# Kernel optimization log

Hardware: AMD Instinct MI355X
Metric: run time of the kernel (lower is better)

## Reference

```python
import jax, jax.numpy as jnp
import numpy as np

N_NODES = 100_000
N_EDGES = 1_600_000
N_GRAPHS = 512
NF = 64        # n_node_feats
H1 = 128       # hidden width
H2 = 64        # dim_node_emb
DIM_OUT = 1
STEPS = 4      # set2set processing steps


def _lin(x, W, b):
    # torch Linear convention: y = x @ W.T + b, W: [out, in]
    return x @ W.T + b


def _gelu(x):
    return jax.nn.gelu(x, approximate=False)  # torch.nn.GELU default (erf)


def _lstm_cell(x, h, c, Wih, Whh, bih, bhh):
    g = x @ Wih.T + bih + h @ Whh.T + bhh
    i, f, gg, o = jnp.split(g, 4, axis=-1)  # torch gate order: i, f, g, o
    i, f, o = jax.nn.sigmoid(i), jax.nn.sigmoid(f), jax.nn.sigmoid(o)
    gg = jnp.tanh(gg)
    c = f * c + i * gg
    h = o * jnp.tanh(c)
    return h, c


def setup_inputs() -> dict:
    key = jax.random.key(0)
    ks = jax.random.split(key, 24)
    p = lambda k, shp: jax.random.normal(k, shp, dtype=jnp.float32) * 0.05
    inp = {
        "x": jax.random.normal(ks[0], (N_NODES, NF), dtype=jnp.float32),
        "edge_index": jax.random.randint(ks[1], (2, N_EDGES), 0, N_NODES, dtype=jnp.int32),
        "batch": jnp.sort(jax.random.randint(ks[2], (N_NODES,), 0, N_GRAPHS, dtype=jnp.int32)),
        "nfc_W": p(ks[3], (H1, NF)), "nfc_b": p(ks[4], (H1,)),
        "gc1_W": p(ks[5], (H1, H1)), "gc1_b": p(ks[6], (H1,)),
        "gc2_W": p(ks[7], (H2, H1)), "gc2_b": p(ks[8], (H2,)),
        "lstm0_Wih": p(ks[9], (4 * H2, 2 * H2)), "lstm0_Whh": p(ks[10], (4 * H2, H2)),
        "lstm0_bih": p(ks[11], (4 * H2,)), "lstm0_bhh": p(ks[12], (4 * H2,)),
        "lstm1_Wih": p(ks[13], (4 * H2, H2)), "lstm1_Whh": p(ks[14], (4 * H2, H2)),
        "lstm1_bih": p(ks[15], (4 * H2,)), "lstm1_bhh": p(ks[16], (4 * H2,)),
        "fc1_W": p(ks[17], (32, 2 * H2)), "fc1_b": p(ks[18], (32,)),
        "fc2_W": p(ks[19], (DIM_OUT, 32)), "fc2_b": p(ks[20], (DIM_OUT,)),
    }
    return inp


def _forward(x, edge_index, batch, nfc_W, nfc_b, gc1_W, gc1_b, gc2_W, gc2_b,
             lstm0_Wih, lstm0_Whh, lstm0_bih, lstm0_bhh,
             lstm1_Wih, lstm1_Whh, lstm1_bih, lstm1_bhh,
             fc1_W, fc1_b, fc2_W, fc2_b):
    src, dst = edge_index[0], edge_index[1]

    def gin_conv(h, W, b):
        # PyG GINConv, eps=0: lin((1+eps)*x + sum_{j in N(i)} x_j)
        agg = jax.ops.segment_sum(h[src], dst, num_segments=N_NODES)
        return _lin(h + agg, W, b)

    h = _gelu(_lin(x, nfc_W, nfc_b))
    h = _gelu(gin_conv(h, gc1_W, gc1_b))
    h = _gelu(gin_conv(h, gc2_W, gc2_b))
    # F.normalize(p=2, dim=1)
    h = h / jnp.maximum(jnp.linalg.norm(h, axis=1, keepdims=True), 1e-12)

    # Set2Set: 2-layer LSTM, 4 processing steps, scatter-softmax attention
    B = N_GRAPHS
    h0 = jnp.zeros((B, H2), jnp.float32); c0 = jnp.zeros((B, H2), jnp.float32)
    h1 = jnp.zeros((B, H2), jnp.float32); c1 = jnp.zeros((B, H2), jnp.float32)
    q_star = jnp.zeros((B, 2 * H2), jnp.float32)
    for _ in range(STEPS):
        h0, c0 = _lstm_cell(q_star, h0, c0, lstm0_Wih, lstm0_Whh, lstm0_bih, lstm0_bhh)
        h1, c1 = _lstm_cell(h0, h1, c1, lstm1_Wih, lstm1_Whh, lstm1_bih, lstm1_bhh)
        q = h1  # [B, H2]
        e = jnp.sum(h * q[batch], axis=-1, keepdims=True)  # [N, 1]
        m = jax.ops.segment_max(e, batch, num_segments=B)
        ex = jnp.exp(e - m[batch])
        s = jax.ops.segment_sum(ex, batch, num_segments=B)
        a = ex / (s[batch] + 1e-16)
        r = jax.ops.segment_sum(a * h, batch, num_segments=B)  # [B, H2]
        q_star = jnp.concatenate([q, r], axis=-1)

    z = _gelu(_lin(q_star, fc1_W, fc1_b))
    z = _lin(z, fc2_W, fc2_b)
    return z, h


def reference(x, edge_index, batch, nfc_W, nfc_b, gc1_W, gc1_b, gc2_W, gc2_b,
              lstm0_Wih, lstm0_Whh, lstm0_bih, lstm0_bhh,
              lstm1_Wih, lstm1_Whh, lstm1_bih, lstm1_bhh,
              fc1_W, fc1_b, fc2_W, fc2_b):
    return _forward(x, edge_index, batch, nfc_W, nfc_b, gc1_W, gc1_b, gc2_W, gc2_b,
                    lstm0_Wih, lstm0_Whh, lstm0_bih, lstm0_bhh,
                    lstm1_Wih, lstm1_Whh, lstm1_bih, lstm1_bhh,
                    fc1_W, fc1_b, fc2_W, fc2_b)
```

## Files before the change

kernel.cpp:

```cpp
#include <hip/hip_runtime.h>
#include <hip/hip_bf16.h>
#include <hip/hip_fp16.h>
#include <math.h>

constexpr int N  = 100000;
constexpr int E  = 1600000;
constexpr int NG = 512;
constexpr int NF = 64;
constexpr int H1 = 128;
constexpr int H2 = 64;

constexpr int BW   = 128;
constexpr int NB   = (N + BW - 1) / BW;
constexpr int CAP  = 2600;
constexpr int CHUNK = 4096;

constexpr int MAXN = 416;
constexpr int RST  = 68;

typedef __attribute__((ext_vector_type(8))) short short8;
typedef __attribute__((ext_vector_type(4))) float f32x4;

__device__ __forceinline__ float gelu_f(float x) {
    return 0.5f * x * (1.0f + erff(x * 0.70710678118654752f));
}
__device__ __forceinline__ float sigmoid_f(float x) {
    return 1.0f / (1.0f + expf(-x));
}
__device__ __forceinline__ float waveAllSum(float v) {
    #pragma unroll
    for (int m = 32; m; m >>= 1) v += __shfl_xor(v, m);
    return v;
}
__device__ __forceinline__ unsigned short f2bf(float x) {
    __hip_bfloat16 b = __float2bfloat16(x);
    return *reinterpret_cast<unsigned short*>(&b);
}
__device__ __forceinline__ float bf2f(unsigned short u) {
    return __uint_as_float(((unsigned int)u) << 16);
}
__device__ __forceinline__ float bf_lo(unsigned int u) { return __uint_as_float(u << 16); }
__device__ __forceinline__ float bf_hi(unsigned int u) { return __uint_as_float(u & 0xffff0000u); }

__device__ __forceinline__ void bfsplit(float v, unsigned short& hi, unsigned short& lo) {
    hi = f2bf(v);
    lo = f2bf(v - bf2f(hi));
}

__device__ __forceinline__ void pack8(float4 a, float4 b, short8& h8, short8& l8) {
    unsigned short h0,h1,h2,h3,h4,h5,h6,h7,l0,l1,l2,l3,l4,l5,l6,l7;
    bfsplit(a.x,h0,l0); bfsplit(a.y,h1,l1); bfsplit(a.z,h2,l2); bfsplit(a.w,h3,l3);
    bfsplit(b.x,h4,l4); bfsplit(b.y,h5,l5); bfsplit(b.z,h6,l6); bfsplit(b.w,h7,l7);
    union { uint4 u; short8 s; } th, tl;
    th.u = make_uint4((unsigned)h0|((unsigned)h1<<16),(unsigned)h2|((unsigned)h3<<16),
                      (unsigned)h4|((unsigned)h5<<16),(unsigned)h6|((unsigned)h7<<16));
    tl.u = make_uint4((unsigned)l0|((unsigned)l1<<16),(unsigned)l2|((unsigned)l3<<16),
                      (unsigned)l4|((unsigned)l5<<16),(unsigned)l6|((unsigned)l7<<16));
    h8 = th.s; l8 = tl.s;
}

__global__ __launch_bounds__(256) void setup_kernel(const int* __restrict__ batch,
                                                    const float* __restrict__ Wih0, const float* __restrict__ Whh0,
                                                    const float* __restrict__ bih0, const float* __restrict__ bhh0,
                                                    const float* __restrict__ Wih1, const float* __restrict__ Whh1,
                                                    const float* __restrict__ bih1, const float* __restrict__ bhh1,
                                                    const float* __restrict__ gc1W, const float* __restrict__ gc2W,
                                                    const float* __restrict__ nfcW,
                                                    float* __restrict__ WT0, float* __restrict__ WT1,
                                                    float* __restrict__ b0, float* __restrict__ b1,
                                                    unsigned short* __restrict__ W1F, unsigned short* __restrict__ W2F,
                                                    unsigned short* __restrict__ W0F,
                                                    int* __restrict__ bcursor, int* __restrict__ gstart) {
    int i = blockIdx.x * 256 + threadIdx.x;
    if (i < 192 * 256) {
        int k = i >> 8, j = i & 255;
        WT0[i] = (k < 128) ? Wih0[j * 128 + k] : Whh0[j * 64 + (k - 128)];
    }
    if (i < 128 * 256) {
        int k = i >> 8, j = i & 255;
        WT1[i] = (k < 64) ? Wih1[j * 64 + k] : Whh1[j * 64 + (k - 64)];
    }
    if (i < 16384) {
        int f = i >> 9, r = i & 511, l = r >> 3, j = r & 7;
        int c = f >> 3, ct = f & 7;
        int o = ct * 16 + (l & 15), k = c * 32 + (l >> 4) * 8 + j;
        unsigned short hi, lo;
        bfsplit(gc1W[o * 128 + k], hi, lo);
        W1F[f * 1024 + r] = hi;
        W1F[f * 1024 + 512 + r] = lo;
    }
    if (i < 8192) {
        int f = i >> 9, r = i & 511, l = r >> 3, j = r & 7;
        int c2 = f >> 2, ct2 = f & 3;
        int o = ct2 * 16 + (l & 15), k = c2 * 32 + (l >> 4) * 8 + j;
        unsigned short hi, lo;
        bfsplit(gc2W[o * 128 + k], hi, lo);
        W2F[f * 1024 + r] = hi;
        W2F[f * 1024 + 512 + r] = lo;
    }
    if (i < 8192) {
        int f = i >> 9, r = i & 511, l = r >> 3, j = r & 7;
        int c = f >> 3, ct = f & 7;
        int o = ct * 16 + (l & 15), k = c * 32 + (l >> 4) * 8 + j;
        unsigned short hi, lo;
        bfsplit(nfcW[o * 64 + k], hi, lo);
        W0F[f * 1024 + r] = hi;
        W0F[f * 1024 + 512 + r] = lo;
    }
    if (i < 256) { b0[i] = bih0[i] + bhh0[i]; b1[i] = bih1[i] + bhh1[i]; }
    if (i < NB) bcursor[i] = i * CAP;
    if (i <= NG) {
        if (i == NG) gstart[NG] = N;
        else {
            int lo = 0, hi = N;
            while (lo < hi) {
                int mid = (lo + hi) >> 1;
                if (batch[mid] < i) lo = mid + 1; else hi = mid;
            }
            gstart[i] = lo;
        }
    }
}

__global__ __launch_bounds__(256) void bin_scatter_kernel(const int* __restrict__ ei,
                                                          int* __restrict__ bcursor,
                                                          int* __restrict__ pairs) {
    __shared__ int hist[NB];
    __shared__ int start_s[NB];
    __shared__ int lcur[NB];
    int tid = threadIdx.x;
    int e0 = blockIdx.x * CHUNK;
    for (int b = tid; b < NB; b += 256) hist[b] = 0;
    __syncthreads();
    #pragma unroll 4
    for (int k = 0; k < CHUNK / 256; ++k) {
        int e = e0 + k * 256 + tid;
        if (e < E) atomicAdd(&hist[ei[E + e] >> 7], 1);
    }
    __syncthreads();
    for (int b = tid; b < NB; b += 256) {
        if (hist[b]) start_s[b] = atomicAdd(&bcursor[b], hist[b]);
        lcur[b] = 0;
    }
    __syncthreads();
    #pragma unroll 4
    for (int k = 0; k < CHUNK / 256; ++k) {
        int e = e0 + k * 256 + tid;
        if (e < E) {
            int d = ei[E + e];
            int s = ei[e];
            int b = d >> 7;
            int pos = start_s[b] + atomicAdd(&lcur[b], 1);
            if (pos < (b + 1) * CAP) pairs[pos] = (s << 7) | (d & 127);
        }
    }
}

__global__ __launch_bounds__(256) void csr_bucket_kernel(const int* __restrict__ pairs,
                                                         const int* __restrict__ bcursor,
                                                         int* __restrict__ srcs,
                                                         int2* __restrict__ nrange) {
    __shared__ int cnt_l[BW];
    __shared__ int cur_l[BW];
    __shared__ int wt[2];
    int b = blockIdx.x;
    int tid = threadIdx.x;
    int base = b * CAP;
    int cnt = bcursor[b] - base;
    if (cnt > CAP) cnt = CAP;
    if (tid < BW) cnt_l[tid] = 0;
    __syncthreads();
    for (int i = tid; i < cnt; i += 256) {
        atomicAdd(&cnt_l[pairs[base + i] & 127], 1);
    }
    __syncthreads();
    if (tid < BW) {
        int v = cnt_l[tid];
        int lane = tid & 63, w = tid >> 6;
        int incl = v;
        #pragma unroll
        for (int off = 1; off < 64; off <<= 1) {
            int t = __shfl_up(incl, off);
            if (lane >= off) incl += t;
        }
        if (lane == 63) wt[w] = incl;
        __syncthreads();
        int excl = (w ? wt[0] : 0) + incl - v;
        int node = b * BW + tid;
        if (node < N) nrange[node] = make_int2(base + excl, base + excl + v);
        cur_l[tid] = excl;
    } else {
        __syncthreads();
    }
    __syncthreads();
    for (int i = tid; i < cnt; i += 256) {
        int p = pairs[base + i];
        int pos = atomicAdd(&cur_l[p & 127], 1);
        srcs[base + pos] = p >> 7;
    }
}

__global__ __launch_bounds__(512, 2) void lin1_kernel(const float* __restrict__ x,
                                                      const uint4* __restrict__ W0F,
                                                      const float* __restrict__ bias,
                                                      unsigned short* __restrict__ out_bf, int nrows) {
    constexpr int EPS = 136;
    __shared__ __align__(16) uint4 w0lds[2048];
    __shared__ __align__(16) unsigned short eps[8][16 * EPS];
    union U8 { uint4 u; short8 s; };
    int tid = threadIdx.x, w = tid >> 6, lane = tid & 63;
    int m15 = lane & 15, quad = lane >> 4;
    int rowbase = blockIdx.x * 128 + w * 16;
    int r0 = rowbase + m15; if (r0 >= nrows) r0 = nrows - 1;

    #pragma unroll
    for (int i = 0; i < 4; ++i) w0lds[i * 512 + tid] = W0F[i * 512 + tid];
    __syncthreads();

    f32x4 acc[8];
    #pragma unroll
    for (int ct = 0; ct < 8; ++ct) acc[ct] = (f32x4)0.f;

    float4 p0[2][2];
    #pragma unroll
    for (int c = 0; c < 2; ++c) {
        p0[c][0] = *(const float4*)&x[(size_t)r0 * 64 + c * 32 + quad * 8];
        p0[c][1] = *(const float4*)&x[(size_t)r0 * 64 + c * 32 + quad * 8 + 4];
    }

    #pragma unroll
    for (int c = 0; c < 2; ++c) {
        short8 ah0, al0;
        pack8(p0[c][0], p0[c][1], ah0, al0);
        #pragma unroll
        for (int ct = 0; ct < 8; ++ct) {
            U8 th, tl;
            th.u = w0lds[(c * 8 + ct) * 128 + lane];
            tl.u = w0lds[(c * 8 + ct) * 128 + 64 + lane];
            short8 bh = th.s, bl = tl.s;
            acc[ct] = __builtin_amdgcn_mfma_f32_16x16x32_bf16(ah0, bh, acc[ct], 0, 0, 0);
            acc[ct] = __builtin_amdgcn_mfma_f32_16x16x32_bf16(ah0, bl, acc[ct], 0, 0, 0);
            acc[ct] = __builtin_amdgcn_mfma_f32_16x16x32_bf16(al0, bh, acc[ct], 0, 0, 0);
        }
    }

    unsigned short* ep = eps[w];
    #pragma unroll
    for (int ct = 0; ct < 8; ++ct) {
        float bc = bias[ct * 16 + m15];
        #pragma unroll
        for (int r = 0; r < 4; ++r) {
            int node = quad * 4 + r;
            ep[node * EPS + ct * 16 + m15] = f2bf(gelu_f(acc[ct][r] + bc));
        }
    }
    asm volatile("s_waitcnt lgkmcnt(0)" ::: "memory");
    #pragma unroll
    for (int it = 0; it < 4; ++it) {
        int idx = it * 64 + lane;
        int rowl = idx >> 4, off = (idx & 15) * 8;
        int grow = rowbase + rowl;
        if (grow < nrows)
            *(uint4*)(out_bf + (size_t)grow * 128 + off) = *(const uint4*)&ep[rowl * EPS + off];
    }
}

__global__ __launch_bounds__(256) void agg_kernel(const uint4* __restrict__ h4,
                                                  const int2* __restrict__ nrange,
                                                  const int* __restrict__ srcs,
                                                  uint4* __restrict__ utab) {
    int wave = threadIdx.x >> 6, lane = threadIdx.x & 63;
    int qw = lane >> 4, ql = lane & 15;
    int n = blockIdx.x * 4 + wave;
    if (n >= N) return;
    int2 rng = nrange[n];
    int s0 = rng.x, deg = rng.y - rng.x;
    int m1 = deg < 64 ? deg : 64;
    int pre = (lane < m1) ? srcs[s0 + lane] : 0;
    float a0 = 0.f, a1 = 0.f, a2 = 0.f, a3 = 0.f, a4 = 0.f, a5 = 0.f, a6 = 0.f, a7 = 0.f;
    auto addu = [&](uint4 u) {
        a0 += bf_lo(u.x); a1 += bf_hi(u.x); a2 += bf_lo(u.y); a3 += bf_hi(u.y);
        a4 += bf_lo(u.z); a5 += bf_hi(u.z); a6 += bf_lo(u.w); a7 += bf_hi(u.w);
    };
    int t = 0;
    for (; t + 16 <= m1; t += 16) {
        int i0 = __shfl(pre, t + qw);
        int i1 = __shfl(pre, t + 4 + qw);
        int i2 = __shfl(pre, t + 8 + qw);
        int i3 = __shfl(pre, t + 12 + qw);
        uint4 u0 = h4[(size_t)i0 * 16 + ql];
        uint4 u1 = h4[(size_t)i1 * 16 + ql];
        uint4 u2 = h4[(size_t)i2 * 16 + ql];
        uint4 u3 = h4[(size_t)i3 * 16 + ql];
        addu(u0); addu(u1); addu(u2); addu(u3);
    }
    for (; t < m1; t += 4) {
        int idx = t + qw;
        int s = __shfl(pre, idx < m1 ? idx : 0);
        if (idx < m1) addu(h4[(size_t)s * 16 + ql]);
    }
    for (int j = 64 + qw; j < deg; j += 4) addu(h4[(size_t)srcs[s0 + j] * 16 + ql]);
    a0 += __shfl_down(a0, 32); a1 += __shfl_down(a1, 32);
    a2 += __shfl_down(a2, 32); a3 += __shfl_down(a3, 32);
    a4 += __shfl_down(a4, 32); a5 += __shfl_down(a5, 32);
    a6 += __shfl_down(a6, 32); a7 += __shfl_down(a7, 32);
    a0 += __shfl_down(a0, 16); a1 += __shfl_down(a1, 16);
    a2 += __shfl_down(a2, 16); a3 += __shfl_down(a3, 16);
    a4 += __shfl_down(a4, 16); a5 += __shfl_down(a5, 16);
    a6 += __shfl_down(a6, 16); a7 += __shfl_down(a7, 16);
    if (qw == 0) {
        addu(h4[(size_t)n * 16 + ql]);
        unsigned short h0, h1, h2, h3, h4_, h5, h6, h7;
        unsigned short l0, l1, l2, l3, l4, l5, l6, l7;
        bfsplit(a0, h0, l0); bfsplit(a1, h1, l1);
        bfsplit(a2, h2, l2); bfsplit(a3, h3, l3);
        bfsplit(a4, h4_, l4); bfsplit(a5, h5, l5);
        bfsplit(a6, h6, l6); bfsplit(a7, h7, l7);
        uint4 o0, o1;
        o0.x = (unsigned)h0 | ((unsigned)h1 << 16);
        o0.y = (unsigned)h2 | ((unsigned)h3 << 16);
        o0.z = (unsigned)l0 | ((unsigned)l1 << 16);
        o0.w = (unsigned)l2 | ((unsigned)l3 << 16);
        o1.x = (unsigned)h4_ | ((unsigned)h5 << 16);
        o1.y = (unsigned)h6 | ((unsigned)h7 << 16);
        o1.z = (unsigned)l4 | ((unsigned)l5 << 16);
        o1.w = (unsigned)l6 | ((unsigned)l7 << 16);
        utab[(size_t)n * 32 + 2 * ql]     = o0;
        utab[(size_t)n * 32 + 2 * ql + 1] = o1;
    }
}

__global__ __launch_bounds__(512, 2) void lin2_fused_kernel(const uint4* __restrict__ in4,
                                                            const uint4* __restrict__ W1F,
                                                            const float* __restrict__ b1,
                                                            const uint4* __restrict__ W2F,
                                                            unsigned short* __restrict__ y2,
                                                            int nrows) {
    constexpr int AST2 = 40;
    __shared__ __align__(16) uint4 wlds[6144];
    __shared__ __align__(16) unsigned short relds[8 * 1280];
    union U8 { uint4 u; short8 s; };
    int tid = threadIdx.x, w = tid >> 6, lane = tid & 63;
    int m15 = lane & 15, quad = lane >> 4;
    unsigned short* myL = relds + w * 1280;
    int rowbase = blockIdx.x * 128 + w * 16;
    int r0 = rowbase + m15; if (r0 >= nrows) r0 = nrows - 1;
    const uint4* a0p = in4 + (size_t)r0 * 32 + quad * 2;

    #pragma unroll
    for (int i = 0; i < 12; ++i) {
        int idx = i * 512 + tid;
        wlds[idx] = (idx < 4096) ? W1F[idx] : W2F[idx - 4096];
    }

    uint4 a[8];
    #pragma unroll
    for (int c = 0; c < 4; ++c) { a[2 * c] = a0p[c * 8]; a[2 * c + 1] = a0p[c * 8 + 1]; }

    float bc[8];
    #pragma unroll
    for (int ct = 0; ct < 8; ++ct) bc[ct] = b1[ct * 16 + m15];

    __syncthreads();
    const uint4* W1L = wlds;
    const uint4* W2L = wlds + 4096;

    f32x4 acc[8];
    #pragma unroll
    for (int ct = 0; ct < 8; ++ct) acc[ct] = (f32x4)0.f;

    #pragma unroll
    for (int c = 0; c < 4; ++c) {
        U8 t;
        uint4 u00 = a[2 * c], u01 = a[2 * c + 1];
        t.u = make_uint4(u00.x, u00.y, u01.x, u01.y); short8 ah0 = t.s;
        t.u = make_uint4(u00.z, u00.w, u01.z, u01.w); short8 al0 = t.s;
        #pragma unroll
        for (int ct = 0; ct < 8; ++ct) {
            U8 th, tl;
            th.u = W1L[(c * 8 + ct) * 128 + lane];
            tl.u = W1L[(c * 8 + ct) * 128 + 64 + lane];
            short8 bh = th.s, bl = tl.s;
            acc[ct] = __builtin_amdgcn_mfma_f32_16x16x32_bf16(ah0, bh, acc[ct], 0, 0, 0);
            acc[ct] = __builtin_amdgcn_mfma_f32_16x16x32_bf16(ah0, bl, acc[ct], 0, 0, 0);
            acc[ct] = __builtin_amdgcn_mfma_f32_16x16x32_bf16(al0, bh, acc[ct], 0, 0, 0);
        }
    }

    #pragma unroll
    for (int ct = 0; ct < 8; ++ct)
        #pragma unroll
        for (int r = 0; r < 4; ++r)
            acc[ct][r] = gelu_f(acc[ct][r] + bc[ct]);

    unsigned short* Ahi2 = myL;
    unsigned short* Alo2 = myL + 16 * AST2;
    f32x4 acc2[4];
    #pragma unroll
    for (int ct = 0; ct < 4; ++ct) acc2[ct] = (f32x4)0.f;

    #pragma unroll
    for (int c2 = 0; c2 < 4; ++c2) {
        #pragma unroll
        for (int cc = 0; cc < 2; ++cc) {
            int ct = c2 * 2 + cc;
            #pragma unroll
            for (int r = 0; r < 4; ++r) {
                int node = quad * 4 + r;
                unsigned short hi, lo;
                bfsplit(acc[ct][r], hi, lo);
                Ahi2[node * AST2 + cc * 16 + m15] = hi;
                Alo2[node * AST2 + cc * 16 + m15] = lo;
            }
        }
        asm volatile("s_waitcnt lgkmcnt(0)" ::: "memory");
        short8 ah0 = *(const short8*)&Ahi2[m15 * AST2 + quad * 8];
        short8 al0 = *(const short8*)&Alo2[m15 * AST2 + quad * 8];
        #pragma unroll
        for (int ct2 = 0; ct2 < 4; ++ct2) {
            U8 th, tl;
            th.u = W2L[(c2 * 4 + ct2) * 128 + lane];
            tl.u = W2L[(c2 * 4 + ct2) * 128 + 64 + lane];
            short8 bh = th.s, bl = tl.s;
            acc2[ct2] = __builtin_amdgcn_mfma_f32_16x16x32_bf16(ah0, bh, acc2[ct2], 0, 0, 0);
            acc2[ct2] = __builtin_amdgcn_mfma_f32_16x16x32_bf16(ah0, bl, acc2[ct2], 0, 0, 0);
            acc2[ct2] = __builtin_amdgcn_mfma_f32_16x16x32_bf16(al0, bh, acc2[ct2], 0, 0, 0);
        }
    }

    unsigned short* ep = myL;
    #pragma unroll
    for (int ct2 = 0; ct2 < 4; ++ct2)
        #pragma unroll
        for (int r = 0; r < 4; ++r) {
            int node = quad * 4 + r;
            __half hv = __float2half(acc2[ct2][r]);
            ep[node * 72 + ct2 * 16 + m15] = *reinterpret_cast<unsigned short*>(&hv);
        }
    asm volatile("s_waitcnt lgkmcnt(0)" ::: "memory");
    #pragma unroll
    for (int it = 0; it < 2; ++it) {
        int idx = it * 64 + lane;
        int rowl = idx >> 3, off = (idx & 7) * 8;
        int grow = rowbase + rowl;
        if (grow < nrows)
            *(uint4*)(y2 + (size_t)grow * 64 + off) = *(const uint4*)&ep[rowl * 72 + off];
    }
}

__global__ __launch_bounds__(256) void agg2_norm_kernel(const uint2* __restrict__ y2,
                                                        const int2* __restrict__ nrange,
                                                        const int* __restrict__ srcs,
                                                        const float* __restrict__ b2,
                                                        float* __restrict__ hn) {
    int wave = threadIdx.x >> 6, lane = threadIdx.x & 63;
    int qw = lane >> 4, ql = lane & 15;
    int n = blockIdx.x * 4 + wave;
    if (n >= N) return;
    int2 rng = nrange[n];
    int s0 = rng.x, deg = rng.y - rng.x;
    int m1 = deg < 64 ? deg : 64;
    int pre = (lane < m1) ? srcs[s0 + lane] : 0;
    float a0 = 0.f, a1 = 0.f, a2 = 0.f, a3 = 0.f;
    auto addu = [&](uint2 u) {
        float2 f01 = __half22float2(*reinterpret_cast<__half2*>(&u.x));
        float2 f23 = __half22float2(*reinterpret_cast<__half2*>(&u.y));
        a0 += f01.x; a1 += f01.y; a2 += f23.x; a3 += f23.y;
    };
    int t = 0;
    for (; t + 16 <= m1; t += 16) {
        int i0 = __shfl(pre, t + qw);
        int i1 = __shfl(pre, t + 4 + qw);
        int i2 = __shfl(pre, t + 8 + qw);
        int i3 = __shfl(pre, t + 12 + qw);
        uint2 u0 = y2[(size_t)i0 * 16 + ql];
        uint2 u1 = y2[(size_t)i1 * 16 + ql];
        uint2 u2 = y2[(size_t)i2 * 16 + ql];
        uint2 u3 = y2[(size_t)i3 * 16 + ql];
        addu(u0); addu(u1); addu(u2); addu(u3);
    }
    for (; t < m1; t += 4) {
        int idx = t + qw;
        int s = __shfl(pre, idx < m1 ? idx : 0);
        if (idx < m1) addu(y2[(size_t)s * 16 + ql]);
    }
    for (int j = 64 + qw; j < deg; j += 4) addu(y2[(size_t)srcs[s0 + j] * 16 + ql]);
    a0 += __shfl_down(a0, 32); a1 += __shfl_down(a1, 32);
    a2 += __shfl_down(a2, 32); a3 += __shfl_down(a3, 32);
    a0 += __shfl_down(a0, 16); a1 += __shfl_down(a1, 16);
    a2 += __shfl_down(a2, 16); a3 += __shfl_down(a3, 16);
    if (qw == 0) {
        addu(y2[(size_t)n * 16 + ql]);
        float4 bv = *(const float4*)&b2[ql * 4];
        float v0 = gelu_f(a0 + bv.x), v1 = gelu_f(a1 + bv.y);
        float v2 = gelu_f(a2 + bv.z), v3 = gelu_f(a3 + bv.w);
        float ss = v0 * v0 + v1 * v1 + v2 * v2 + v3 * v3;
        #pragma unroll
        for (int mm = 1; mm < 16; mm <<= 1) ss += __shfl_xor(ss, mm);
        float d = fmaxf(sqrtf(ss), 1e-12f);
        *(float4*)&hn[(size_t)n * 64 + ql * 4] = make_float4(v0 / d, v1 / d, v2 / d, v3 / d);
    }
}

__global__ __launch_bounds__(256) void set2set_kernel(const float* __restrict__ hn,
                                                      const int* __restrict__ gstart,
                                                      const float* __restrict__ WT0, const float* __restrict__ b0,
                                                      const float* __restrict__ WT1, const float* __restrict__ b1,
                                                      const float* __restrict__ fc1W, const float* __restrict__ fc1b,
                                                      const float* __restrict__ fc2W, const float* __restrict__ fc2b,
                                                      float* __restrict__ zout) {
    __shared__ __align__(16) unsigned short hL[MAXN * RST];
    __shared__ float av[MAXN];
    __shared__ __align__(16) float xc0[192];
    __shared__ __align__(16) float xc1[128];
    __shared__ __align__(16) float gates[256];
    __shared__ float c0v[H2], c1v[H2];
    __shared__ float red[4];
    __shared__ float rp[4][H2];
    __shared__ float sp[4];
    __shared__ float fcWT[128 * 32];

    int g = blockIdx.x;
    int tid = threadIdx.x, w = tid >> 6, lane = tid & 63;
    int s0 = gstart[g], s1 = gstart[g + 1];
    int cnt = s1 - s0;
    int cL = cnt < MAXN ? cnt : MAXN;
    const float* hq = xc1 + 64;

    for (int idx = tid; idx < cL * 16; idx += 256) {
        int n = idx >> 4, p4 = idx & 15;
        float4 v = *(const float4*)&hn[(size_t)(s0 + n) * 64 + p4 * 4];
        uint2 u;
        u.x = (unsigned int)f2bf(v.x) | ((unsigned int)f2bf(v.y) << 16);
        u.y = (unsigned int)f2bf(v.z) | ((unsigned int)f2bf(v.w) << 16);
        *(uint2*)&hL[n * RST + p4 * 4] = u;
    }
    for (int i = tid; i < 4096; i += 256) {
        int j = i >> 7, k = i & 127;
        fcWT[k * 32 + j] = fc1W[i];
    }
    if (tid < 192) xc0[tid] = 0.f;
    if (tid < 128) xc1[tid] = 0.f;
    if (tid < H2) { c0v[tid] = 0.f; c1v[tid] = 0.f; }
    float b0v = b0[tid], b1v = b1[tid];
    __syncthreads();

    for (int step = 0; step < 4; ++step) {
        {
            float a0 = 0.f, a1 = 0.f, a2 = 0.f, a3 = 0.f;
            #pragma unroll 8
            for (int k = 0; k < 192; k += 4) {
                a0 += xc0[k]     * WT0[(k)     * 256 + tid];
                a1 += xc0[k + 1] * WT0[(k + 1) * 256 + tid];
                a2 += xc0[k + 2] * WT0[(k + 2) * 256 + tid];
                a3 += xc0[k + 3] * WT0[(k + 3) * 256 + tid];
            }
            gates[tid] = (a0 + a1) + (a2 + a3) + b0v;
        }
        __syncthreads();
        if (tid < H2) {
            float ii = sigmoid_f(gates[tid]), ff = sigmoid_f(gates[H2 + tid]);
            float gg = tanhf(gates[2 * H2 + tid]), oo = sigmoid_f(gates[3 * H2 + tid]);
            float c = ff * c0v[tid] + ii * gg;
            float h = oo * tanhf(c);
            c0v[tid] = c; xc0[128 + tid] = h; xc1[tid] = h;
        }
        __syncthreads();
        {
            float a0 = 0.f, a1 = 0.f, a2 = 0.f, a3 = 0.f;
            #pragma unroll 8
            for (int k = 0; k < 128; k += 4) {
                a0 += xc1[k]     * WT1[(k)     * 256 + tid];
                a1 += xc1[k + 1] * WT1[(k + 1) * 256 + tid];
                a2 += xc1[k + 2] * WT1[(k + 2) * 256 + tid];
                a3 += xc1[k + 3] * WT1[(k + 3) * 256 + tid];
            }
            gates[tid] = (a0 + a1) + (a2 + a3) + b1v;
        }
        __syncthreads();
        if (tid < H2) {
            float ii = sigmoid_f(gates[tid]), ff = sigmoid_f(gates[H2 + tid]);
            float gg = tanhf(gates[2 * H2 + tid]), oo = sigmoid_f(gates[3 * H2 + tid]);
            float c = ff * c1v[tid] + ii * gg;
            float h = oo * tanhf(c);
            c1v[tid] = c; xc1[64 + tid] = h;
        }
        __syncthreads();

        float lm = -INFINITY;
        for (int i = tid; i < cnt; i += 256) {
            float e = 0.f;
            if (i < MAXN) {
                const uint2* row = (const uint2*)&hL[i * RST];
                #pragma unroll
                for (int p4 = 0; p4 < 16; ++p4) {
                    uint2 u = row[p4];
                    e += bf_lo(u.x) * hq[p4 * 4 + 0];
                    e += bf_hi(u.x) * hq[p4 * 4 + 1];
                    e += bf_lo(u.y) * hq[p4 * 4 + 2];
                    e += bf_hi(u.y) * hq[p4 * 4 + 3];
                }
                av[i] = e;
            } else {
                for (int f = 0; f < 64; ++f) e += hn[(size_t)(s0 + i) * 64 + f] * hq[f];
            }
            lm = fmaxf(lm, e);
        }
        #pragma unroll
        for (int mm = 32; mm; mm >>= 1) lm = fmaxf(lm, __shfl_xor(lm, mm));
        if (lane == 0) red[w] = lm;
        __syncthreads();
        float m = fmaxf(fmaxf(red[0], red[1]), fmaxf(red[2], red[3]));

        float ps = 0.f;
        for (int i = tid; i < cnt; i += 256) {
            float e;
            if (i < MAXN) e = av[i];
            else {
                e = 0.f;
                for (int f = 0; f < 64; ++f) e += hn[(size_t)(s0 + i) * 64 + f] * hq[f];
            }
            float p = expf(e - m);
            ps += p;
            if (i < MAXN) av[i] = p;
        }
        ps = waveAllSum(ps);
        if (lane == 0) sp[w] = ps;
        __syncthreads();
        float s = sp[0] + sp[1] + sp[2] + sp[3];

        float racc = 0.f;
        for (int i = w; i < cL; i += 4) {
            unsigned short hv = hL[i * RST + lane];
            racc += av[i] * bf2f(hv);
        }
        float qf = hq[lane];
        for (int n = MAXN + w; n < cnt; n += 4) {
            float v = hn[(size_t)(s0 + n) * 64 + lane];
            float e = waveAllSum(v * qf);
            float p = expf(e - m);
            racc += p * v;
        }
        rp[w][lane] = racc;
        __syncthreads();
        if (tid < H2) {
            float r = 0.f;
            if (cnt > 0) {
                r = (rp[0][tid] + rp[1][tid] + rp[2][tid] + rp[3][tid]) / (s + 1e-16f);
            }
            xc0[tid] = xc1[64 + tid];
            xc0[H2 + tid] = r;
        }
        __syncthreads();
    }

    if (w == 0) {
        float zv = 0.f;
        if (lane < 32) {
            float a = fc1b[lane];
            #pragma unroll 8
            for (int k = 0; k < 128; ++k) a += xc0[k] * fcWT[k * 32 + lane];
            zv = gelu_f(a) * fc2W[lane];
        }
        zv = waveAllSum(zv);
        if (lane == 0) zout[g] = zv + fc2b[0];
    }
}

extern "C" void kernel_launch(void* const* d_in, const int* in_sizes, int n_in,
                              void* d_out, int out_size, void* d_ws, size_t ws_size,
                              hipStream_t stream) {
    const float* x       = (const float*)d_in[0];
    const int*   ei      = (const int*)d_in[1];
    const int*   batch   = (const int*)d_in[2];
    const float* nfc_W   = (const float*)d_in[3];
    const float* nfc_b   = (const float*)d_in[4];
    const float* gc1_W   = (const float*)d_in[5];
    const float* gc1_b   = (const float*)d_in[6];
    const float* gc2_W   = (const float*)d_in[7];
    const float* gc2_b   = (const float*)d_in[8];
    const float* l0_Wih  = (const float*)d_in[9];
    const float* l0_Whh  = (const float*)d_in[10];
    const float* l0_bih  = (const float*)d_in[11];
    const float* l0_bhh  = (const float*)d_in[12];
    const float* l1_Wih  = (const float*)d_in[13];
    const float* l1_Whh  = (const float*)d_in[14];
    const float* l1_bih  = (const float*)d_in[15];
    const float* l1_bhh  = (const float*)d_in[16];
    const float* fc1_W   = (const float*)d_in[17];
    const float* fc1_b   = (const float*)d_in[18];
    const float* fc2_W   = (const float*)d_in[19];
    const float* fc2_b   = (const float*)d_in[20];

    float* out = (float*)d_out;
    float* hn_out = out + NG;

    char* p = (char*)d_ws;
    auto take = [&](size_t bytes) {
        char* r = p;
        p += (bytes + 255) & ~size_t(255);
        return r;
    };
    float*          sbuf  = (float*)take((size_t)N * H1 * 4);
    unsigned short* hbbuf = (unsigned short*)take((size_t)N * H1 * 2);
    int*   srcs   = (int*)take((size_t)NB * CAP * 4);
    int2*  nrange = (int2*)take((size_t)N * 8);
    int*   bcursor= (int*)take((size_t)NB * 4);
    int*   gstart = (int*)take((size_t)(NG + 1) * 4);
    float* WT0    = (float*)take((size_t)192 * 256 * 4);
    float* WT1    = (float*)take((size_t)128 * 256 * 4);
    float* b0     = (float*)take((size_t)256 * 4);
    float* b1     = (float*)take((size_t)256 * 4);
    unsigned short* W1F = (unsigned short*)take((size_t)32 * 1024 * 2);
    unsigned short* W2F = (unsigned short*)take((size_t)16 * 1024 * 2);
    unsigned short* W0F = (unsigned short*)take((size_t)16 * 1024 * 2);

    int* pairs = (int*)sbuf;

    setup_kernel<<<192, 256, 0, stream>>>(batch, l0_Wih, l0_Whh, l0_bih, l0_bhh,
                                          l1_Wih, l1_Whh, l1_bih, l1_bhh,
                                          gc1_W, gc2_W, nfc_W,
                                          WT0, WT1, b0, b1, W1F, W2F, W0F, bcursor, gstart);

    bin_scatter_kernel<<<(E + CHUNK - 1) / CHUNK, 256, 0, stream>>>(ei, bcursor, pairs);
    csr_bucket_kernel<<<NB, 256, 0, stream>>>(pairs, bcursor, srcs, nrange);

    int linGrid = (N + 127) / 128;
    lin1_kernel<<<linGrid, 512, 0, stream>>>(x, (const uint4*)W0F, nfc_b, hbbuf, N);
    agg_kernel<<<(N + 3) / 4, 256, 0, stream>>>((const uint4*)hbbuf, nrange, srcs, (uint4*)sbuf);
    lin2_fused_kernel<<<linGrid, 512, 0, stream>>>((const uint4*)sbuf, (const uint4*)W1F, gc1_b,
                                                   (const uint4*)W2F, hbbuf, N);
    agg2_norm_kernel<<<(N + 3) / 4, 256, 0, stream>>>((const uint2*)hbbuf, nrange, srcs,
                                                      gc2_b, hn_out);

    set2set_kernel<<<NG, 256, 0, stream>>>(hn_out, gstart, WT0, b0, WT1, b1,
                                           fc1_W, fc1_b, fc2_W, fc2_b, out);
}
```

Before: 392.2 us.

## Widen set2set to 512 threads with register-resident LSTM weights split over K

Result: slower. 576.8 us (+47.1%).

```diff
diff --git a/kernel.cpp b/kernel.cpp
--- a/kernel.cpp
+++ b/kernel.cpp
@@ -502,32 +502,41 @@
     }
 }
 
-__global__ __launch_bounds__(256) void set2set_kernel(const float* __restrict__ hn,
-                                                      const int* __restrict__ gstart,
-                                                      const float* __restrict__ WT0, const float* __restrict__ b0,
-                                                      const float* __restrict__ WT1, const float* __restrict__ b1,
-                                                      const float* __restrict__ fc1W, const float* __restrict__ fc1b,
-                                                      const float* __restrict__ fc2W, const float* __restrict__ fc2b,
-                                                      float* __restrict__ zout) {
+__global__ __launch_bounds__(512, 4) void set2set_kernel(const float* __restrict__ hn,
+                                                         const int* __restrict__ gstart,
+                                                         const float* __restrict__ WT0, const float* __restrict__ b0,
+                                                         const float* __restrict__ WT1, const float* __restrict__ b1,
+                                                         const float* __restrict__ fc1W, const float* __restrict__ fc1b,
+                                                         const float* __restrict__ fc2W, const float* __restrict__ fc2b,
+                                                         float* __restrict__ zout) {
     __shared__ __align__(16) unsigned short hL[MAXN * RST];
     __shared__ float av[MAXN];
     __shared__ __align__(16) float xc0[192];
     __shared__ __align__(16) float xc1[128];
     __shared__ __align__(16) float gates[256];
     __shared__ float c0v[H2], c1v[H2];
-    __shared__ float red[4];
-    __shared__ float rp[4][H2];
-    __shared__ float sp[4];
-    __shared__ float fcWT[128 * 32];
+    __shared__ float red[8];
+    __shared__ float rp[8][H2];
+    __shared__ float sp[8];
+    __shared__ unsigned short fcWTb[128 * 32];
+    __shared__ float psum[512];
 
     int g = blockIdx.x;
     int tid = threadIdx.x, w = tid >> 6, lane = tid & 63;
+    int gg = tid & 255, hh = tid >> 8;
     int s0 = gstart[g], s1 = gstart[g + 1];
     int cnt = s1 - s0;
     int cL = cnt < MAXN ? cnt : MAXN;
     const float* hq = xc1 + 64;
 
-    for (int idx = tid; idx < cL * 16; idx += 256) {
+    float W0reg[96];
+    #pragma unroll
+    for (int k = 0; k < 96; ++k) W0reg[k] = WT0[(hh * 96 + k) * 256 + gg];
+    float W1reg[64];
+    #pragma unroll
+    for (int k = 0; k < 64; ++k) W1reg[k] = WT1[(hh * 64 + k) * 256 + gg];
+
+    for (int idx = tid; idx < cL * 16; idx += 512) {
         int n = idx >> 4, p4 = idx & 15;
         float4 v = *(const float4*)&hn[(size_t)(s0 + n) * 64 + p4 * 4];
         uint2 u;
@@ -535,60 +544,62 @@
         u.y = (unsigned int)f2bf(v.z) | ((unsigned int)f2bf(v.w) << 16);
         *(uint2*)&hL[n * RST + p4 * 4] = u;
     }
-    for (int i = tid; i < 4096; i += 256) {
+    for (int i = tid; i < 4096; i += 512) {
         int j = i >> 7, k = i & 127;
-        fcWT[k * 32 + j] = fc1W[i];
+        fcWTb[k * 32 + j] = f2bf(fc1W[i]);
     }
     if (tid < 192) xc0[tid] = 0.f;
     if (tid < 128) xc1[tid] = 0.f;
     if (tid < H2) { c0v[tid] = 0.f; c1v[tid] = 0.f; }
-    float b0v = b0[tid], b1v = b1[tid];
+    float bb0 = b0[gg], bb1 = b1[gg];
     __syncthreads();
 
     for (int step = 0; step < 4; ++step) {
         {
-            float a0 = 0.f, a1 = 0.f, a2 = 0.f, a3 = 0.f;
-            #pragma unroll 8
-            for (int k = 0; k < 192; k += 4) {
-                a0 += xc0[k]     * WT0[(k)     * 256 + tid];
-                a1 += xc0[k + 1] * WT0[(k + 1) * 256 + tid];
-                a2 += xc0[k + 2] * WT0[(k + 2) * 256 + tid];
-                a3 += xc0[k + 3] * WT0[(k + 3) * 256 + tid];
+            float p = 0.f;
+            #pragma unroll
+            for (int kk = 0; kk < 24; ++kk) {
+                float4 q4 = *(const float4*)&xc0[hh * 96 + kk * 4];
+                p += q4.x * W0reg[4 * kk]     + q4.y * W0reg[4 * kk + 1]
+                   + q4.z * W0reg[4 * kk + 2] + q4.w * W0reg[4 * kk + 3];
             }
-            gates[tid] = (a0 + a1) + (a2 + a3) + b0v;
-        }
+            psum[tid] = p;
+        }
+        __syncthreads();
+        if (tid < 256) gates[tid] = psum[tid] + psum[tid + 256] + bb0;
         __syncthreads();
         if (tid < H2) {
             float ii = sigmoid_f(gates[tid]), ff = sigmoid_f(gates[H2 + tid]);
-            float gg = tanhf(gates[2 * H2 + tid]), oo = sigmoid_f(gates[3 * H2 + tid]);
-            float c = ff * c0v[tid] + ii * gg;
+            float gv = tanhf(gates[2 * H2 + tid]), oo = sigmoid_f(gates[3 * H2 + tid]);
+            float c = ff * c0v[tid] + ii * gv;
             float h = oo * tanhf(c);
             c0v[tid] = c; xc0[128 + tid] = h; xc1[tid] = h;
         }
         __syncthreads();
         {
-            float a0 = 0.f, a1 = 0.f, a2 = 0.f, a3 = 0.f;
-            #pragma unroll 8
-            for (int k = 0; k < 128; k += 4) {
-                a0 += xc1[k]     * WT1[(k)     * 256 + tid];
-                a1 += xc1[k + 1] * WT1[(k + 1) * 256 + tid];
-                a2 += xc1[k + 2] * WT1[(k + 2) * 256 + tid];
-                a3 += xc1[k + 3] * WT1[(k + 3) * 256 + tid];
+            float p = 0.f;
+            #pragma unroll
+            for (int kk = 0; kk < 16; ++kk) {
+                float4 q4 = *(const float4*)&xc1[hh * 64 + kk * 4];
+                p += q4.x * W1reg[4 * kk]     + q4.y * W1reg[4 * kk + 1]
+                   + q4.z * W1reg[4 * kk + 2] + q4.w * W1reg[4 * kk + 3];
             }
-            gates[tid] = (a0 + a1) + (a2 + a3) + b1v;
-        }
+            psum[tid] = p;
+        }
+        __syncthreads();
+        if (tid < 256) gates[tid] = psum[tid] + psum[tid + 256] + bb1;
         __syncthreads();
         if (tid < H2) {
             float ii = sigmoid_f(gates[tid]), ff = sigmoid_f(gates[H2 + tid]);
-            float gg = tanhf(gates[2 * H2 + tid]), oo = sigmoid_f(gates[3 * H2 + tid]);
-            float c = ff * c1v[tid] + ii * gg;
+            float gv = tanhf(gates[2 * H2 + tid]), oo = sigmoid_f(gates[3 * H2 + tid]);
+            float c = ff * c1v[tid] + ii * gv;
             float h = oo * tanhf(c);
             c1v[tid] = c; xc1[64 + tid] = h;
         }
         __syncthreads();
 
         float lm = -INFINITY;
-        for (int i = tid; i < cnt; i += 256) {
+        for (int i = tid; i < cnt; i += 512) {
             float e = 0.f;
             if (i < MAXN) {
                 const uint2* row = (const uint2*)&hL[i * RST];
@@ -610,10 +621,12 @@
         for (int mm = 32; mm; mm >>= 1) lm = fmaxf(lm, __shfl_xor(lm, mm));
         if (lane == 0) red[w] = lm;
         __syncthreads();
-        float m = fmaxf(fmaxf(red[0], red[1]), fmaxf(red[2], red[3]));
+        float m = red[0];
+        #pragma unroll
+        for (int j = 1; j < 8; ++j) m = fmaxf(m, red[j]);
 
         float ps = 0.f;
-        for (int i = tid; i < cnt; i += 256) {
+        for (int i = tid; i < cnt; i += 512) {
             float e;
             if (i < MAXN) e = av[i];
             else {
@@ -627,15 +640,17 @@
         ps = waveAllSum(ps);
         if (lane == 0) sp[w] = ps;
         __syncthreads();
-        float s = sp[0] + sp[1] + sp[2] + sp[3];
+        float s = 0.f;
+        #pragma unroll
+        for (int j = 0; j < 8; ++j) s += sp[j];
 
         float racc = 0.f;
-        for (int i = w; i < cL; i += 4) {
+        for (int i = w; i < cL; i += 8) {
             unsigned short hv = hL[i * RST + lane];
             racc += av[i] * bf2f(hv);
         }
         float qf = hq[lane];
-        for (int n = MAXN + w; n < cnt; n += 4) {
+        for (int n = MAXN + w; n < cnt; n += 8) {
             float v = hn[(size_t)(s0 + n) * 64 + lane];
             float e = waveAllSum(v * qf);
             float p = expf(e - m);
@@ -646,7 +661,10 @@
         if (tid < H2) {
             float r = 0.f;
             if (cnt > 0) {
-                r = (rp[0][tid] + rp[1][tid] + rp[2][tid] + rp[3][tid]) / (s + 1e-16f);
+                float rs = rp[0][tid];
+                #pragma unroll
+                for (int j = 1; j < 8; ++j) rs += rp[j][tid];
+                r = rs / (s + 1e-16f);
             }
             xc0[tid] = xc1[64 + tid];
             xc0[H2 + tid] = r;
@@ -659,7 +677,7 @@
         if (lane < 32) {
             float a = fc1b[lane];
             #pragma unroll 8
-            for (int k = 0; k < 128; ++k) a += xc0[k] * fcWT[k * 32 + lane];
+            for (int k = 0; k < 128; ++k) a += xc0[k] * bf2f(fcWTb[k * 32 + lane]);
             zv = gelu_f(a) * fc2W[lane];
         }
         zv = waveAllSum(zv);
@@ -733,6 +751,6 @@
     agg2_norm_kernel<<<(N + 3) / 4, 256, 0, stream>>>((const uint2*)hbbuf, nrange, srcs,
                                                       gc2_b, hn_out);
 
-    set2set_kernel<<<NG, 256, 0, stream>>>(hn_out, gstart, WT0, b0, WT1, b1,
+    set2set_kernel<<<NG, 512, 0, stream>>>(hn_out, gstart, WT0, b0, WT1, b1,
                                            fc1_W, fc1_b, fc2_W, fc2_b, out);
 }
```
